# Kernel tuning notes

Measured on AMD Instinct MI355X. Metric: run time of the kernel, lower is better.

Reference implementation:

```python
import jax, jax.numpy as jnp
import numpy as np

GROUPS = 32
EPS = 1e-5


def setup_inputs() -> dict:
    key = jax.random.key(0)
    ks = jax.random.split(key, 6)
    B, H, W, C = 2, 64, 64, 512
    wscale = 0.02  # keep logits in a sane range for softmax
    return {
        "x": jax.random.normal(ks[0], (B, H, W, C), dtype=jnp.float32),
        "gamma": jnp.ones((C,), jnp.float32),
        "beta": jnp.zeros((C,), jnp.float32),
        "wq": jax.random.normal(ks[1], (C, C), dtype=jnp.float32) * wscale,
        "bq": jnp.zeros((C,), jnp.float32),
        "wk": jax.random.normal(ks[2], (C, C), dtype=jnp.float32) * wscale,
        "bk": jnp.zeros((C,), jnp.float32),
        "wv": jax.random.normal(ks[3], (C, C), dtype=jnp.float32) * wscale,
        "bv": jnp.zeros((C,), jnp.float32),
        "wp": jax.random.normal(ks[4], (C, C), dtype=jnp.float32) * wscale,
        "bp": jnp.zeros((C,), jnp.float32),
    }


def _group_norm(x, gamma, beta):
    B, H, W, C = x.shape
    xg = x.reshape(B, H, W, GROUPS, C // GROUPS)
    mean = xg.mean(axis=(1, 2, 4), keepdims=True)
    var = xg.var(axis=(1, 2, 4), keepdims=True)
    xn = ((xg - mean) * jax.lax.rsqrt(var + EPS)).reshape(B, H, W, C)
    return xn * gamma + beta


def reference(x, gamma, beta, wq, bq, wk, bk, wv, bv, wp, bp):
    B, H, W, C = x.shape
    xn = _group_norm(x, gamma, beta)
    # 1x1 convs == per-pixel linear layers
    q = (xn @ wq + bq).reshape(B, H * W, C)
    k = (xn @ wk + bk).reshape(B, H * W, C)
    v = (xn @ wv + bv).reshape(B, H * W, C)
    scale = C ** (-0.5)
    attn = jax.nn.softmax(jnp.einsum("bqc,bkc->bqk", q, k) * scale, axis=-1)
    out = jnp.einsum("bqk,bkc->bqc", attn, v).reshape(B, H, W, C)
    return (out @ wp + bp) + x
```

## Files before the change

### kernel.cpp

```cpp
#include <hip/hip_runtime.h>


typedef __bf16 bf16_t;
typedef __bf16 bf16x8 __attribute__((ext_vector_type(8)));
typedef __bf16 bf16x4 __attribute__((ext_vector_type(4)));
typedef float  f32x4  __attribute__((ext_vector_type(4)));

__device__ __forceinline__ bf16x8 ld8(const bf16_t* p) {
    return *reinterpret_cast<const bf16x8*>(p);
}
__device__ __forceinline__ f32x4 mfma16(bf16x8 a, bf16x8 b, f32x4 c) {
    return __builtin_amdgcn_mfma_f32_16x16x32_bf16(a, b, c, 0, 0, 0);
}
__device__ __forceinline__ void gload16(const bf16_t* gp, bf16_t* lp) {
    __builtin_amdgcn_global_load_lds(
        (const __attribute__((address_space(1))) void*)gp,
        (__attribute__((address_space(3))) void*)lp, 16, 0, 0);
}

#define NPIX 8192
#define C512 512
#define SEQ  4096
#define QSCALE 0.044194173824159216f

__global__ __launch_bounds__(256) void gn_sum_k(const float* __restrict__ x,
                                                float* __restrict__ accum) {
    int bg    = blockIdx.x >> 3;
    int slice = blockIdx.x & 7;
    int b = bg >> 5, g = bg & 31;
    const float* xp = x + (size_t)b * SEQ * C512 + g * 16;
    float s = 0.f, s2 = 0.f;
    #pragma unroll
    for (int pp = 0; pp < 2; pp++) {
        int p = slice * 512 + pp * 256 + threadIdx.x;
        const float4* q = reinterpret_cast<const float4*>(xp + (size_t)p * C512);
        #pragma unroll
        for (int i = 0; i < 4; i++) {
            float4 v = q[i];
            s  += v.x + v.y + v.z + v.w;
            s2 += v.x*v.x + v.y*v.y + v.z*v.z + v.w*v.w;
        }
    }
    #pragma unroll
    for (int off = 32; off >= 1; off >>= 1) {
        s  += __shfl_down(s, off);
        s2 += __shfl_down(s2, off);
    }
    __shared__ float rs[4], rs2[4];
    int wave = threadIdx.x >> 6;
    if ((threadIdx.x & 63) == 0) { rs[wave] = s; rs2[wave] = s2; }
    __syncthreads();
    if (threadIdx.x == 0) {
        float S = rs[0] + rs[1] + rs[2] + rs[3];
        float S2 = rs2[0] + rs2[1] + rs2[2] + rs2[3];
        atomicAdd(&accum[bg * 2],     S);
        atomicAdd(&accum[bg * 2 + 1], S2);
    }
}

__global__ __launch_bounds__(256) void wt_conv_k(const float* wq, const float* wk,
                                                 const float* wv, const float* wp,
                                                 bf16_t* wqkvT, bf16_t* wpT) {
    int y = blockIdx.y;
    const float* w = (y == 0) ? wq : (y == 1) ? wk : (y == 2) ? wv : wp;
    float scale = (y == 0) ? QSCALE : 1.0f;
    int tid = blockIdx.x * 256 + threadIdx.x;
    int n = tid >> 9, k = tid & 511;
    bf16_t val = (bf16_t)(w[(size_t)k * C512 + n] * scale);
    if (y < 3) wqkvT[((size_t)y * C512 + n) * C512 + k] = val;
    else       wpT[(size_t)n * C512 + k] = val;
}

__global__ __launch_bounds__(256) void bias_merge_k(const float* bq, const float* bk,
                                                    const float* bv, float* bqkv) {
    int i = blockIdx.x * 256 + threadIdx.x;
    float v = (i < 512) ? bq[i] * QSCALE : (i < 1024) ? bk[i - 512] : bv[i - 1024];
    bqkv[i] = v;
}

__global__ __launch_bounds__(256) void xn_k(const float* __restrict__ x,
                                            const float* __restrict__ accum,
                                            const float* __restrict__ gamma,
                                            const float* __restrict__ beta,
                                            bf16_t* __restrict__ xn) {
    size_t idx = ((size_t)blockIdx.x * 256 + threadIdx.x) * 4;
    int c = (int)(idx & 511);
    size_t pix = idx >> 9;
    int b = (int)(pix >> 12);
    int g = c >> 4;
    float sum = accum[(b * 32 + g) * 2];
    float ssq = accum[(b * 32 + g) * 2 + 1];
    float mean = sum * (1.f / 65536.f);
    float var  = ssq * (1.f / 65536.f) - mean * mean;
    float rstd = rsqrtf(var + 1e-5f);
    float4 v  = *reinterpret_cast<const float4*>(x + idx);
    float4 gm = *reinterpret_cast<const float4*>(gamma + c);
    float4 bt = *reinterpret_cast<const float4*>(beta + c);
    bf16x4 o;
    o[0] = (bf16_t)((v.x - mean) * rstd * gm.x + bt.x);
    o[1] = (bf16_t)((v.y - mean) * rstd * gm.y + bt.y);
    o[2] = (bf16_t)((v.z - mean) * rstd * gm.z + bt.z);
    o[3] = (bf16_t)((v.w - mean) * rstd * gm.w + bt.w);
    *reinterpret_cast<bf16x4*>(xn + idx) = o;
}

template <int MODE>
__global__ __launch_bounds__(256, 2) void gemm128_k(
        const bf16_t* __restrict__ Aall, const bf16_t* __restrict__ Ball,
        const float* __restrict__ bias, const float* __restrict__ resid,
        void* __restrict__ out0, void* __restrict__ out1,
        void* __restrict__ out2, void* __restrict__ out3,
        float* __restrict__ lsum) {
    constexpr int TM  = (MODE == 3) ? 64 : 128;
    constexpr int ASZ = TM * 32;
    constexpr int ACH = TM / 16;
    constexpr int CPW = (ACH + 8) / 4;
    constexpr int MI  = TM / 32;
    __shared__ bf16_t smem[2 * ASZ + 8192];

    int lane = threadIdx.x & 63;
    int w    = threadIdx.x >> 6;
    int wr   = w >> 1, wc = w & 1;
    int lrow = lane & 15, quad = lane >> 4;

    const bf16_t* A = Aall;
    const bf16_t* B = Ball;
    size_t lda = 512, ldb = 512;
    int ksteps = 16;

    int bm = blockIdx.x * TM, bn = blockIdx.y * 128;

    auto stage = [&](int buf, int ks) {
        size_t k0 = (size_t)ks * 32;
        #pragma unroll
        for (int ii = 0; ii < CPW; ii++) {
            int c = w * CPW + ii;
            if (c < ACH) {
                const bf16_t* gpA = A + (size_t)(bm + c * 16 + lrow) * lda + k0 + quad * 8;
                gload16(gpA, &smem[buf * ASZ + c * 512]);
            } else {
                int cb = c - ACH;
                const bf16_t* gpB = B + (size_t)(bn + cb * 16 + lrow) * ldb + k0 + quad * 8;
                gload16(gpB, &smem[2 * ASZ + buf * 4096 + cb * 512]);
            }
        }
    };

    f32x4 acc[MI][4] = {};

    stage(0, 0);

    for (int ks = 0; ks < ksteps; ks++) {
        int cur = ks & 1;
        __syncthreads();
        if (ks + 1 < ksteps) stage(1 - cur, ks + 1);

        const bf16_t* al = &smem[cur * ASZ + (wr * MI) * 512];
        const bf16_t* bl = &smem[2 * ASZ + cur * 4096 + (wc * 4) * 512];
        bf16x8 af[MI], bf[4];
        #pragma unroll
        for (int m = 0; m < MI; m++) af[m] = ld8(al + m * 512 + lane * 8);
        #pragma unroll
        for (int n = 0; n < 4; n++) bf[n] = ld8(bl + n * 512 + lane * 8);
        #pragma unroll
        for (int m = 0; m < MI; m++)
            #pragma unroll
            for (int n = 0; n < 4; n++)
                acc[m][n] = mfma16(af[m], bf[n], acc[m][n]);
    }

    #pragma unroll
    for (int m = 0; m < MI; m++) {
        int rowb = bm + wr * (TM / 2) + m * 16 + quad * 4;
        #pragma unroll
        for (int n = 0; n < 4; n++) {
            int col = bn + wc * 64 + n * 16 + lrow;
            #pragma unroll
            for (int i = 0; i < 4; i++) {
                int row = rowb + i;
                float v = acc[m][n][i];
                if (MODE == 0) {
                    int seg = col >> 9, c = col & 511;
                    bf16_t val = (bf16_t)(v + bias[col]);
                    if (seg == 0) {
                        ((bf16_t*)out0)[(size_t)row * C512 + c] = val;
                    } else if (seg == 1) {
                        ((bf16_t*)out1)[(size_t)row * C512 + c] = val;
                    } else {
                        int b = row >> 12, s = row & 4095;
                        ((bf16_t*)out2)[((size_t)(b * C512 + c)) * SEQ + s] = val;
                    }
                } else {
                    size_t idx = (size_t)row * C512 + col;
                    ((float*)out0)[idx] = v + bias[col] + resid[idx];
                }
            }
        }
    }
}

__global__ __launch_bounds__(512, 1) void fattn_k(
        const bf16_t* __restrict__ Q, const bf16_t* __restrict__ K,
        const bf16_t* __restrict__ VT, bf16_t* __restrict__ Op0,
        bf16_t* __restrict__ Op1, float* __restrict__ lsum) {
    __shared__ bf16_t Kl[2][32 * 512];
    __shared__ bf16_t Vl[2][512 * 32];
    __shared__ bf16_t Pl[64 * 32];

    int bid = blockIdx.x;
    int xcd = bid & 7, loc = bid >> 3;
    int b   = (xcd >> 1) & 1;
    int kv  = xcd & 1;
    int q0  = ((xcd >> 2) * 32 + loc) * 64;
    int key0 = kv * 2048;

    const bf16_t* Qb = Q  + (size_t)b * SEQ * C512;
    const bf16_t* Kb = K  + (size_t)b * SEQ * C512;
    const bf16_t* Vb = VT + (size_t)b * C512 * SEQ;
    bf16_t* Op = kv ? Op1 : Op0;

    int lane = threadIdx.x & 63;
    int w    = threadIdx.x >> 6;
    int lrow = lane & 15, quad = lane >> 4;
    int qt = w & 3, kt = w >> 2;

    bf16x8 qf[16];
    const bf16_t* qp = Qb + (size_t)(q0 + qt * 16 + lrow) * C512 + quad * 8;
    #pragma unroll
    for (int ks = 0; ks < 16; ks++) qf[ks] = ld8(qp + ks * 32);

    auto stage = [&](int buf, int t) {
        #pragma unroll
        for (int ii = 0; ii < 8; ii++) {
            int cc = w * 8 + ii;
            if (cc < 32) {
                int ks = cc >> 1, ktc = cc & 1;
                const bf16_t* gp = Kb +
                    (size_t)(key0 + t * 32 + ktc * 16 + lrow) * C512 + ks * 32 + quad * 8;
                gload16(gp, &Kl[buf][cc * 512]);
            } else {
                int ct = cc - 32;
                const bf16_t* gp = Vb +
                    (size_t)(ct * 16 + lrow) * SEQ + key0 + t * 32 + quad * 8;
                gload16(gp, &Vl[buf][ct * 512]);
            }
        }
    };

    f32x4 oacc[4][4] = {};
    float rs[4] = {0.f, 0.f, 0.f, 0.f};

    stage(0, 0);

    for (int t = 0; t < 64; t++) {
        int cur = t & 1;
        __syncthreads();
        if (t < 63) stage(cur ^ 1, t + 1);

        f32x4 sa = {0.f, 0.f, 0.f, 0.f};
        #pragma unroll
        for (int ks = 0; ks < 16; ks++) {
            bf16x8 bf = ld8(&Kl[cur][(ks * 2 + kt) * 512 + lane * 8]);
            sa = mfma16(qf[ks], bf, sa);
        }
        #pragma unroll
        for (int i = 0; i < 4; i++) {
            float p = __expf(fminf(sa[i], 20.0f));
            rs[i] += p;
            int off = qt * 512 + (quad * 4 + i) * 8 +
                      (kt * 2 + (lrow >> 3)) * 128 + (lrow & 7);
            Pl[off] = (bf16_t)p;
        }
        asm volatile("s_waitcnt lgkmcnt(0)" ::: "memory");
        __builtin_amdgcn_s_barrier();
        __builtin_amdgcn_sched_barrier(0);

        bf16x8 pa[4];
        #pragma unroll
        for (int m = 0; m < 4; m++) pa[m] = ld8(&Pl[m * 512 + lane * 8]);
        #pragma unroll
        for (int n = 0; n < 4; n++) {
            bf16x8 vf = ld8(&Vl[cur][(w * 4 + n) * 512 + lane * 8]);
            #pragma unroll
            for (int m = 0; m < 4; m++)
                oacc[m][n] = mfma16(pa[m], vf, oacc[m][n]);
        }
    }

    #pragma unroll
    for (int i = 0; i < 4; i++) {
        float r = rs[i];
        r += __shfl_xor(r, 1);
        r += __shfl_xor(r, 2);
        r += __shfl_xor(r, 4);
        r += __shfl_xor(r, 8);
        if (lrow == 0)
            atomicAdd(&lsum[(size_t)b * SEQ + q0 + qt * 16 + quad * 4 + i], r);
    }

    #pragma unroll
    for (int m = 0; m < 4; m++) {
        int row = q0 + m * 16 + quad * 4;
        #pragma unroll
        for (int n = 0; n < 4; n++) {
            int col = w * 64 + n * 16 + lrow;
            #pragma unroll
            for (int i = 0; i < 4; i++)
                Op[((size_t)b * SEQ + row + i) * C512 + col] = (bf16_t)oacc[m][n][i];
        }
    }
}

__global__ __launch_bounds__(256) void attn_combine2_k(
        const bf16_t* __restrict__ Op0, const bf16_t* __restrict__ Op1,
        const float* __restrict__ lsum, bf16_t* __restrict__ O) {
    int idx = blockIdx.x * 256 + threadIdx.x;
    int row = idx >> 6;
    int c8  = (idx & 63) << 3;
    float inv = 1.0f / lsum[row];
    size_t base = (size_t)row * C512 + c8;
    bf16x8 o0 = ld8(Op0 + base), o1 = ld8(Op1 + base);
    bf16x8 o;
    #pragma unroll
    for (int j = 0; j < 8; j++)
        o[j] = (bf16_t)(((float)o0[j] + (float)o1[j]) * inv);
    *reinterpret_cast<bf16x8*>(O + base) = o;
}

extern "C" void kernel_launch(void* const* d_in, const int* in_sizes, int n_in,
                              void* d_out, int out_size, void* d_ws, size_t ws_size,
                              hipStream_t stream) {
    const float* x     = (const float*)d_in[0];
    const float* gamma = (const float*)d_in[1];
    const float* beta  = (const float*)d_in[2];
    const float* wq = (const float*)d_in[3];  const float* bq = (const float*)d_in[4];
    const float* wk = (const float*)d_in[5];  const float* bk = (const float*)d_in[6];
    const float* wv = (const float*)d_in[7];  const float* bv = (const float*)d_in[8];
    const float* wp = (const float*)d_in[9];  const float* bp = (const float*)d_in[10];
    float* out = (float*)d_out;

    char* ws = (char*)d_ws;
    size_t off = 0;
    float*  bqkv   = (float*)(ws + off);   off += 1536 * sizeof(float);
    float*  lsum   = (float*)(ws + off);   off += (size_t)NPIX * sizeof(float);
    float*  accum  = (float*)(ws + off);   off += 128 * sizeof(float);
    bf16_t* xn     = (bf16_t*)(ws + off);  off += (size_t)NPIX * C512 * 2;
    bf16_t* wqkvT  = (bf16_t*)(ws + off);  off += (size_t)3 * C512 * C512 * 2;
    bf16_t* wpT    = (bf16_t*)(ws + off);  off += (size_t)C512 * C512 * 2;
    bf16_t* Qb     = (bf16_t*)(ws + off);  off += (size_t)NPIX * C512 * 2;
    bf16_t* Kb     = (bf16_t*)(ws + off);  off += (size_t)NPIX * C512 * 2;
    bf16_t* VTb    = (bf16_t*)(ws + off);  off += (size_t)NPIX * C512 * 2;
    bf16_t* Op0    = (bf16_t*)(ws + off);  off += (size_t)NPIX * C512 * 2;
    bf16_t* Op1    = (bf16_t*)(ws + off);  off += (size_t)NPIX * C512 * 2;
    bf16_t* Ob  = xn;

    hipMemsetAsync(lsum, 0, (size_t)(NPIX + 128) * sizeof(float), stream);

    gn_sum_k<<<512, 256, 0, stream>>>(x, accum);
    wt_conv_k<<<dim3(1024, 4), 256, 0, stream>>>(wq, wk, wv, wp, wqkvT, wpT);
    bias_merge_k<<<6, 256, 0, stream>>>(bq, bk, bv, bqkv);
    xn_k<<<4096, 256, 0, stream>>>(x, accum, gamma, beta, xn);

    gemm128_k<0><<<dim3(64, 12, 1), 256, 0, stream>>>(
        xn, wqkvT, bqkv, nullptr, Qb, Kb, VTb, nullptr, nullptr);

    fattn_k<<<256, 512, 0, stream>>>(Qb, Kb, VTb, Op0, Op1, lsum);

    attn_combine2_k<<<2048, 256, 0, stream>>>(Op0, Op1, lsum, Ob);

    gemm128_k<3><<<dim3(128, 4, 1), 256, 0, stream>>>(
        Ob, wpT, bp, x, out, nullptr, nullptr, nullptr, nullptr);
}
```

Measured before the change: 305.3 us.

## Fuse split-KV combine into projection GEMM and merge bias kernel into weight conversion

Drops the separate attention-combine kernel. The output-projection GEMM now reads both partial outputs, Op0 and Op1, as a doubled K dimension (32 k-steps) and applies the 1/lsum normalization in its epilogue, which works because the row scaling commutes with the projection. The bias-merge kernel is folded into the weight-conversion kernel as an extra grid row, saving a launch. The attention QK loop is split into two independent MFMA accumulator chains and wrapped in s_setprio raises to favour the matrix instructions, at the cost of doubling the projection GEMM's K work.

Measured after the change: 304.5 us. Within noise of the previous version (-0.3%).

```diff
diff --git a/kernel.cpp b/kernel.cpp
--- a/kernel.cpp
+++ b/kernel.cpp
@@ -60,8 +60,18 @@
 
 __global__ __launch_bounds__(256) void wt_conv_k(const float* wq, const float* wk,
                                                  const float* wv, const float* wp,
-                                                 bf16_t* wqkvT, bf16_t* wpT) {
+                                                 const float* bq, const float* bk,
+                                                 const float* bv,
+                                                 bf16_t* wqkvT, bf16_t* wpT,
+                                                 float* bqkv) {
     int y = blockIdx.y;
+    if (y == 4) {
+        if (blockIdx.x >= 6) return;
+        int i = blockIdx.x * 256 + threadIdx.x;
+        float v = (i < 512) ? bq[i] * QSCALE : (i < 1024) ? bk[i - 512] : bv[i - 1024];
+        bqkv[i] = v;
+        return;
+    }
     const float* w = (y == 0) ? wq : (y == 1) ? wk : (y == 2) ? wv : wp;
     float scale = (y == 0) ? QSCALE : 1.0f;
     int tid = blockIdx.x * 256 + threadIdx.x;
@@ -69,13 +79,6 @@
     bf16_t val = (bf16_t)(w[(size_t)k * C512 + n] * scale);
     if (y < 3) wqkvT[((size_t)y * C512 + n) * C512 + k] = val;
     else       wpT[(size_t)n * C512 + k] = val;
-}
-
-__global__ __launch_bounds__(256) void bias_merge_k(const float* bq, const float* bk,
-                                                    const float* bv, float* bqkv) {
-    int i = blockIdx.x * 256 + threadIdx.x;
-    float v = (i < 512) ? bq[i] * QSCALE : (i < 1024) ? bk[i - 512] : bv[i - 1024];
-    bqkv[i] = v;
 }
 
 __global__ __launch_bounds__(256) void xn_k(const float* __restrict__ x,
@@ -123,20 +126,22 @@
     int wr   = w >> 1, wc = w & 1;
     int lrow = lane & 15, quad = lane >> 4;
 
-    const bf16_t* A = Aall;
-    const bf16_t* B = Ball;
+    const bf16_t* A  = Aall;
+    const bf16_t* A1 = (MODE == 3) ? (const bf16_t*)out1 : nullptr;
+    const bf16_t* B  = Ball;
     size_t lda = 512, ldb = 512;
-    int ksteps = 16;
+    int ksteps = (MODE == 3) ? 32 : 16;
 
     int bm = blockIdx.x * TM, bn = blockIdx.y * 128;
 
     auto stage = [&](int buf, int ks) {
-        size_t k0 = (size_t)ks * 32;
+        const bf16_t* Ap = (MODE == 3 && ks >= 16) ? A1 : A;
+        size_t k0 = (size_t)(MODE == 3 ? (ks & 15) : ks) * 32;
         #pragma unroll
         for (int ii = 0; ii < CPW; ii++) {
             int c = w * CPW + ii;
             if (c < ACH) {
-                const bf16_t* gpA = A + (size_t)(bm + c * 16 + lrow) * lda + k0 + quad * 8;
+                const bf16_t* gpA = Ap + (size_t)(bm + c * 16 + lrow) * lda + k0 + quad * 8;
                 gload16(gpA, &smem[buf * ASZ + c * 512]);
             } else {
                 int cb = c - ACH;
@@ -192,7 +197,8 @@
                     }
                 } else {
                     size_t idx = (size_t)row * C512 + col;
-                    ((float*)out0)[idx] = v + bias[col] + resid[idx];
+                    float inv = 1.0f / lsum[row];
+                    ((float*)out0)[idx] = v * inv + bias[col] + resid[idx];
                 }
             }
         }
@@ -255,14 +261,19 @@
     for (int t = 0; t < 64; t++) {
         int cur = t & 1;
         __syncthreads();
-        if (t < 63) stage(cur ^ 1, t + 1);
-
-        f32x4 sa = {0.f, 0.f, 0.f, 0.f};
-        #pragma unroll
-        for (int ks = 0; ks < 16; ks++) {
-            bf16x8 bf = ld8(&Kl[cur][(ks * 2 + kt) * 512 + lane * 8]);
-            sa = mfma16(qf[ks], bf, sa);
-        }
+        if (t < 63) stage(1 - cur, t + 1);
+
+        f32x4 sa0 = {}, sa1 = {};
+        __builtin_amdgcn_s_setprio(1);
+        #pragma unroll
+        for (int ks = 0; ks < 8; ks++) {
+            bf16x8 kf0 = ld8(&Kl[cur][((2 * ks) * 2 + kt) * 512 + lane * 8]);
+            bf16x8 kf1 = ld8(&Kl[cur][((2 * ks + 1) * 2 + kt) * 512 + lane * 8]);
+            sa0 = mfma16(qf[2 * ks],     kf0, sa0);
+            sa1 = mfma16(qf[2 * ks + 1], kf1, sa1);
+        }
+        __builtin_amdgcn_s_setprio(0);
+        f32x4 sa = sa0 + sa1;
         #pragma unroll
         for (int i = 0; i < 4; i++) {
             float p = __expf(fminf(sa[i], 20.0f));
@@ -278,6 +289,7 @@
         bf16x8 pa[4];
         #pragma unroll
         for (int m = 0; m < 4; m++) pa[m] = ld8(&Pl[m * 512 + lane * 8]);
+        __builtin_amdgcn_s_setprio(1);
         #pragma unroll
         for (int n = 0; n < 4; n++) {
             bf16x8 vf = ld8(&Vl[cur][(w * 4 + n) * 512 + lane * 8]);
@@ -285,6 +297,7 @@
             for (int m = 0; m < 4; m++)
                 oacc[m][n] = mfma16(pa[m], vf, oacc[m][n]);
         }
+        __builtin_amdgcn_s_setprio(0);
     }
 
     #pragma unroll
@@ -309,22 +322,6 @@
                 Op[((size_t)b * SEQ + row + i) * C512 + col] = (bf16_t)oacc[m][n][i];
         }
     }
-}
-
-__global__ __launch_bounds__(256) void attn_combine2_k(
-        const bf16_t* __restrict__ Op0, const bf16_t* __restrict__ Op1,
-        const float* __restrict__ lsum, bf16_t* __restrict__ O) {
-    int idx = blockIdx.x * 256 + threadIdx.x;
-    int row = idx >> 6;
-    int c8  = (idx & 63) << 3;
-    float inv = 1.0f / lsum[row];
-    size_t base = (size_t)row * C512 + c8;
-    bf16x8 o0 = ld8(Op0 + base), o1 = ld8(Op1 + base);
-    bf16x8 o;
-    #pragma unroll
-    for (int j = 0; j < 8; j++)
-        o[j] = (bf16_t)(((float)o0[j] + (float)o1[j]) * inv);
-    *reinterpret_cast<bf16x8*>(O + base) = o;
 }
 
 extern "C" void kernel_launch(void* const* d_in, const int* in_sizes, int n_in,
@@ -352,13 +349,12 @@
     bf16_t* VTb    = (bf16_t*)(ws + off);  off += (size_t)NPIX * C512 * 2;
     bf16_t* Op0    = (bf16_t*)(ws + off);  off += (size_t)NPIX * C512 * 2;
     bf16_t* Op1    = (bf16_t*)(ws + off);  off += (size_t)NPIX * C512 * 2;
-    bf16_t* Ob  = xn;
 
     hipMemsetAsync(lsum, 0, (size_t)(NPIX + 128) * sizeof(float), stream);
 
     gn_sum_k<<<512, 256, 0, stream>>>(x, accum);
-    wt_conv_k<<<dim3(1024, 4), 256, 0, stream>>>(wq, wk, wv, wp, wqkvT, wpT);
-    bias_merge_k<<<6, 256, 0, stream>>>(bq, bk, bv, bqkv);
+    wt_conv_k<<<dim3(1024, 5), 256, 0, stream>>>(wq, wk, wv, wp, bq, bk, bv,
+                                                 wqkvT, wpT, bqkv);
     xn_k<<<4096, 256, 0, stream>>>(x, accum, gamma, beta, xn);
 
     gemm128_k<0><<<dim3(64, 12, 1), 256, 0, stream>>>(
@@ -366,8 +362,6 @@
 
     fattn_k<<<256, 512, 0, stream>>>(Qb, Kb, VTb, Op0, Op1, lsum);
 
-    attn_combine2_k<<<2048, 256, 0, stream>>>(Op0, Op1, lsum, Ob);
-
     gemm128_k<3><<<dim3(128, 4, 1), 256, 0, stream>>>(
-        Ob, wpT, bp, x, out, nullptr, nullptr, nullptr, nullptr);
-}
+        Op0, wpT, bp, x, out, Op1, nullptr, nullptr, lsum);
+}
```
